# Optimization experiments

Measured on AMD Instinct MI355X. Metric: run time of the kernel, lower is better.

The kernel has to match this reference:

```python
import jax, jax.numpy as jnp
import numpy as np

B, S, DIM, H = 2, 2048, 1536, 12
HD = DIM // H  # 128
EPS = 1e-6


def setup_inputs() -> dict:
    key = jax.random.key(0)
    ks = jax.random.split(key, 6)
    x = jax.random.normal(ks[0], (B, S, DIM), dtype=jnp.float32)
    # RoPE rotation as (cos, sin) pairs: shape [S, 1, HD//2, 2]
    inv = 1.0 / (10000.0 ** (np.arange(0, HD, 2, dtype=np.float32) / HD))
    ang = np.arange(S, dtype=np.float32)[:, None] * inv[None, :]  # [S, HD//2]
    freqs = jnp.asarray(np.stack([np.cos(ang), np.sin(ang)], axis=-1))[:, None, :, :]
    def lin(k):
        return jax.random.normal(k, (DIM, DIM), dtype=jnp.float32) * 0.02
    wq, wk, wv, wo = lin(ks[1]), lin(ks[2]), lin(ks[3]), lin(ks[4])
    zb = jnp.zeros((DIM,), dtype=jnp.float32)
    ones = jnp.ones((DIM,), dtype=jnp.float32)
    return dict(x=x, freqs=freqs,
                wq=wq, bq=zb, wk=wk, bk=zb, wv=wv, bv=zb, wo=wo, bo=zb,
                gq=ones, gk=ones, timestep=500)


def reference(x, freqs, wq, bq, wk, bk, wv, bv, wo, bo, gq, gk, timestep):
    b, s, dim = x.shape

    def rms(z, g):
        zf = z.astype(jnp.float32)
        n = zf * jax.lax.rsqrt(jnp.mean(zf * zf, axis=-1, keepdims=True) + EPS)
        return n.astype(z.dtype) * g

    def rope(t):
        # [b,s,dim] -> [b,s,H,HD//2,2] pairs; complex multiply by freqs
        tp = t.reshape(b, s, H, HD // 2, 2)
        tr, ti = tp[..., 0], tp[..., 1]
        fr = freqs[None, ..., 0]  # [1,s,1,HD//2] broadcasts over batch & heads
        fi = freqs[None, ..., 1]
        out = jnp.stack([tr * fr - ti * fi, tr * fi + ti * fr], axis=-1)
        return out.reshape(b, s, dim)

    q = rope(rms(x @ wq.T + bq, gq))
    k = rope(rms(x @ wk.T + bk, gk))
    v = x @ wv.T + bv

    qh = q.reshape(b, s, H, HD).transpose(0, 2, 1, 3)
    kh = k.reshape(b, s, H, HD).transpose(0, 2, 1, 3)
    vh = v.reshape(b, s, H, HD).transpose(0, 2, 1, 3)
    scores = jnp.einsum('bhqd,bhkd->bhqk', qh, kh) / np.float32(np.sqrt(HD))
    attn = jax.nn.softmax(scores, axis=-1)
    out = jnp.einsum('bhqk,bhkd->bhqd', attn, vh)
    out = out.transpose(0, 2, 1, 3).reshape(b, s, dim)
    return out @ wo.T + bo
```

## Files before the change

kernel.cpp:

```cpp
#include <hip/hip_runtime.h>
#include <hip/hip_bf16.h>


#define BQ  2
#define SQ  2048
#define DIMQ 1536
#define HQ  12
#define HDQ 128
#define MTOK 4096
#define KDIM 1536

typedef __attribute__((ext_vector_type(8))) short short8;
typedef __attribute__((ext_vector_type(4))) float f32x4;
typedef __attribute__((ext_vector_type(16))) float f32x16;
typedef __attribute__((ext_vector_type(8))) unsigned short u16x8;

typedef __attribute__((address_space(1))) const void global_cvoid;
typedef __attribute__((address_space(3))) void lds_void;

__device__ __forceinline__ float bf2f(unsigned int u) {
    return __uint_as_float(u << 16);
}
__device__ __forceinline__ unsigned short f2bf(float f) {
    unsigned int u = __float_as_uint(f);
    u += 0x7fffu + ((u >> 16) & 1u);
    return (unsigned short)(u >> 16);
}
__device__ __forceinline__ void gload_lds16(const void* g, void* l) {
    __builtin_amdgcn_global_load_lds((global_cvoid*)g, (lds_void*)l, 16, 0, 0);
}
__device__ __forceinline__ unsigned int cvtpk_bf16(float lo, float hi) {
    unsigned int r;
    asm("v_cvt_pk_bf16_f32 %0, %1, %2" : "=v"(r) : "v"(lo), "v"(hi));
    return r;
}

#define VMCNT(n) asm volatile("s_waitcnt vmcnt(" #n ")" ::: "memory")
#define BARRIER() do { asm volatile("" ::: "memory"); \
                       __builtin_amdgcn_s_barrier();  \
                       asm volatile("" ::: "memory"); } while (0)

__global__ __launch_bounds__(256)
void cast_all(const float* __restrict__ x,
              const float* __restrict__ wq, const float* __restrict__ wk,
              const float* __restrict__ wv, const float* __restrict__ wo,
              unsigned short* __restrict__ Xb,
              unsigned short* __restrict__ Wqkv,
              unsigned short* __restrict__ Wob)
{
    const int NX = 1572864, NW = 589824;
    int i = blockIdx.x * blockDim.x + threadIdx.x;
    int stride = gridDim.x * blockDim.x;
    for (; i < NX + 4 * NW; i += stride) {
        const float* s; unsigned short* d; int off;
        if (i < NX) { s = x; d = Xb; off = i; }
        else {
            int j = i - NX;
            int seg = j / NW;
            off = j - seg * NW;
            s = (seg == 0) ? wq : (seg == 1) ? wk : (seg == 2) ? wv : wo;
            d = (seg < 3) ? (Wqkv + seg * 2359296) : Wob;
        }
        float4 v = ((const float4*)s)[off];
        unsigned short a = f2bf(v.x), b = f2bf(v.y), c = f2bf(v.z), e = f2bf(v.w);
        unsigned int lo = (unsigned int)a | ((unsigned int)b << 16);
        unsigned int hi = (unsigned int)c | ((unsigned int)e << 16);
        ((uint2*)d)[off] = make_uint2(lo, hi);
    }
}

template<int MODE>
__global__ __launch_bounds__(256)
void gemm_bt(const unsigned short* __restrict__ A,
             const unsigned short* __restrict__ Bm,
             unsigned short* __restrict__ oQ,
             unsigned short* __restrict__ oK,
             unsigned short* __restrict__ oV,
             const float* __restrict__ biasq,
             const float* __restrict__ biask,
             const float* __restrict__ biasv,
             float* __restrict__ oF,
             const float* __restrict__ biaso)
{
    __shared__ unsigned short ldsA[128 * 64];
    __shared__ unsigned short ldsB[128 * 64];
    const int m0 = blockIdx.x * 128;
    const int n0 = blockIdx.y * 128;
    const int t = threadIdx.x;
    const int lane = t & 63;
    const int wid = t >> 6;
    const int wr = (wid >> 1) * 64;
    const int wc = (wid & 1) * 64;
    const int lr = lane & 15;
    const int lk = lane >> 4;

    f32x4 acc[4][4] = {};

    #pragma unroll 1
    for (int kt = 0; kt < KDIM; kt += 64) {
        #pragma unroll
        for (int i = 0; i < 4; ++i) {
            const int off = i * 4096 + wid * 1024 + lane * 16;
            const int r = off >> 7;
            const int c = (off >> 4) & 7;
            const int csw = (c ^ (r & 7)) << 3;
            gload_lds16(A + (size_t)(m0 + r) * KDIM + kt + csw,
                        (char*)ldsA + i * 4096 + wid * 1024);
            gload_lds16(Bm + (size_t)(n0 + r) * KDIM + kt + csw,
                        (char*)ldsB + i * 4096 + wid * 1024);
        }
        __syncthreads();

        #pragma unroll
        for (int kk = 0; kk < 2; ++kk) {
            short8 af[4], bf[4];
            #pragma unroll
            for (int mi = 0; mi < 4; ++mi) {
                int row = wr + mi * 16 + lr;
                int ch = (kk * 4 + lk) ^ (row & 7);
                af[mi] = *(const short8*)((const char*)ldsA + row * 128 + ch * 16);
            }
            #pragma unroll
            for (int ni = 0; ni < 4; ++ni) {
                int row = wc + ni * 16 + lr;
                int ch = (kk * 4 + lk) ^ (row & 7);
                bf[ni] = *(const short8*)((const char*)ldsB + row * 128 + ch * 16);
            }
            #pragma unroll
            for (int mi = 0; mi < 4; ++mi)
                #pragma unroll
                for (int ni = 0; ni < 4; ++ni)
                    acc[mi][ni] = __builtin_amdgcn_mfma_f32_16x16x32_bf16(
                        af[mi], bf[ni], acc[mi][ni], 0, 0, 0);
        }
        __syncthreads();
    }

    if (MODE == 0) {
        const int seg = n0 / 1536;
        unsigned short* op = (seg == 0) ? oQ : (seg == 1 ? oK : oV);
        const float* bp = (seg == 0) ? biasq : (seg == 1 ? biask : biasv);
        const int nl0 = n0 - seg * 1536;
        #pragma unroll
        for (int mi = 0; mi < 4; ++mi)
            #pragma unroll
            for (int ni = 0; ni < 4; ++ni)
                #pragma unroll
                for (int j = 0; j < 4; ++j) {
                    int row = m0 + wr + mi * 16 + lk * 4 + j;
                    int col = nl0 + wc + ni * 16 + lr;
                    op[(size_t)row * 1536 + col] = f2bf(acc[mi][ni][j] + bp[col]);
                }
    } else {
        #pragma unroll
        for (int mi = 0; mi < 4; ++mi)
            #pragma unroll
            for (int ni = 0; ni < 4; ++ni)
                #pragma unroll
                for (int j = 0; j < 4; ++j) {
                    int row = m0 + wr + mi * 16 + lk * 4 + j;
                    int col = n0 + wc + ni * 16 + lr;
                    oF[(size_t)row * 1536 + col] = acc[mi][ni][j] + biaso[col];
                }
    }
}

__global__ __launch_bounds__(256)
void rmsnorm_rope(unsigned short* __restrict__ T,
                  const float* __restrict__ g,
                  const float* __restrict__ freqs)
{
    const int token = blockIdx.x;
    const int s = token & (SQ - 1);
    unsigned int* row = (unsigned int*)(T + (size_t)token * DIMQ);
    const int t = threadIdx.x;
    const int lane = t & 63, wid = t >> 6;

    float pr[3], pi[3];
    float ss = 0.f;
    #pragma unroll
    for (int q = 0; q < 3; ++q) {
        unsigned int v = row[t + q * 256];
        float a = bf2f(v & 0xffffu);
        float b = bf2f(v >> 16);
        pr[q] = a; pi[q] = b;
        ss += a * a + b * b;
    }
    ss += __shfl_xor(ss, 32); ss += __shfl_xor(ss, 16); ss += __shfl_xor(ss, 8);
    ss += __shfl_xor(ss, 4);  ss += __shfl_xor(ss, 2);  ss += __shfl_xor(ss, 1);
    __shared__ float red[4];
    if (lane == 0) red[wid] = ss;
    __syncthreads();
    float tot = red[0] + red[1] + red[2] + red[3];
    float sc = rsqrtf(tot * (1.0f / 1536.0f) + 1e-6f);

    #pragma unroll
    for (int q = 0; q < 3; ++q) {
        int p = t + q * 256;
        int ph = p & 63;
        float fr = freqs[s * 128 + ph * 2];
        float fi = freqs[s * 128 + ph * 2 + 1];
        float nr = pr[q] * sc * g[2 * p];
        float ni = pi[q] * sc * g[2 * p + 1];
        float outr = nr * fr - ni * fi;
        float outi = nr * fi + ni * fr;
        row[p] = (unsigned int)f2bf(outr) | ((unsigned int)f2bf(outi) << 16);
    }
}

__global__ __launch_bounds__(256)
void vtrans(const unsigned short* __restrict__ V, unsigned short* __restrict__ Vt)
{
    __shared__ unsigned short tile[64][72];
    const int s0 = blockIdx.x * 64;
    const int d0 = blockIdx.y * 64;
    const int bh = blockIdx.z;
    const int b = bh / HQ, h = bh % HQ;
    const int t = threadIdx.x;

    #pragma unroll
    for (int i = 0; i < 2; ++i) {
        int cid = i * 256 + t;
        int r = cid >> 3, c = cid & 7;
        u16x8 v = *(const u16x8*)(V + (size_t)(b * SQ + s0 + r) * DIMQ + h * HDQ + d0 + c * 8);
        #pragma unroll
        for (int e = 0; e < 8; ++e) tile[r][c * 8 + e] = v[e];
    }
    __syncthreads();
    #pragma unroll
    for (int i = 0; i < 2; ++i) {
        int cid = i * 256 + t;
        int rd = cid >> 3, c = cid & 7;
        u16x8 w;
        #pragma unroll
        for (int e = 0; e < 8; ++e) w[e] = tile[c * 8 + e][rd];
        *(u16x8*)(Vt + (size_t)(bh * HDQ + d0 + rd) * SQ + s0 + c * 8) = w;
    }
}

__global__ __launch_bounds__(128)
void attn(const unsigned short* __restrict__ Q,
          const unsigned short* __restrict__ Kb,
          const unsigned short* __restrict__ Vt,
          unsigned short* __restrict__ Ao)
{
    __shared__ char smem[49152];
    char* Kl0 = smem;
    char* Kl1 = smem + 16384;
    char* Vl  = smem + 32768;

    const int fid = blockIdx.x;
    const int xcd = fid & 7;
    const int slot = fid >> 3;
    const int bh = xcd * 3 + (slot >> 5);
    const int sblk = slot & 31;
    const int b = bh / HQ, h = bh % HQ;
    const int s0 = sblk * 64;

    const int t = threadIdx.x;
    const int lane = t & 63, wid = t >> 6;
    const int l31 = lane & 31, hi = lane >> 5;
    const float THR = 90.5f;
    const float CE = 0.12751879f;

    const unsigned short* Kbase = Kb + (size_t)(b * SQ) * DIMQ + h * HDQ;
    const unsigned short* Vbase = Vt + (size_t)(bh * HDQ) * SQ;

    short8 qf[8];
    {
        const int qrow = b * SQ + s0 + wid * 32 + l31;
        const unsigned short* qp = Q + (size_t)qrow * DIMQ + h * HDQ;
        #pragma unroll
        for (int kc = 0; kc < 8; ++kc)
            qf[kc] = *(const short8*)(qp + kc * 16 + hi * 8);
    }

    float mrun = -1e30f, lsum = 0.f;
    f32x16 oacc[4] = {};

    #pragma unroll
    for (int i = 0; i < 8; ++i) {
        const int off = i * 2048 + t * 16;
        int r = off >> 8, c = (off >> 4) & 15;
        gload_lds16(Kbase + (size_t)r * DIMQ + ((c ^ (r & 7)) << 3),
                    Kl0 + i * 2048 + wid * 1024);
    }

    char* kcur = Kl0;
    char* knxt = Kl1;

    #pragma unroll 1
    for (int kv0 = 0; kv0 < SQ; kv0 += 64) {
        #pragma unroll
        for (int i = 0; i < 8; ++i) {
            const int off = i * 2048 + t * 16;
            int r = off >> 7, c = (off >> 4) & 7;
            gload_lds16(Vbase + (size_t)r * SQ + kv0 + ((c ^ (r & 7)) << 3),
                        Vl + i * 2048 + wid * 1024);
        }
        asm volatile("" ::: "memory");
        const int kvn = (kv0 + 64 < SQ) ? kv0 + 64 : kv0;
        #pragma unroll
        for (int i = 0; i < 8; ++i) {
            const int off = i * 2048 + t * 16;
            int r = off >> 8, c = (off >> 4) & 15;
            gload_lds16(Kbase + (size_t)(kvn + r) * DIMQ + ((c ^ (r & 7)) << 3),
                        knxt + i * 2048 + wid * 1024);
        }

        VMCNT(16);
        BARRIER();

        f32x16 sacc[2] = {};
        __builtin_amdgcn_s_setprio(1);
        #pragma unroll
        for (int kvt = 0; kvt < 2; ++kvt) {
            const int krow = kvt * 32 + l31;
            const int rb = krow * 256;
            #pragma unroll
            for (int kc = 0; kc < 8; ++kc) {
                int ch = (kc * 2 + hi) ^ (krow & 7);
                short8 kf = *(const short8*)(kcur + rb + ch * 16);
                sacc[kvt] = __builtin_amdgcn_mfma_f32_32x32x16_bf16(kf, qf[kc], sacc[kvt], 0, 0, 0);
            }
        }
        __builtin_amdgcn_s_setprio(0);

        float mt[16];
        #pragma unroll
        for (int r = 0; r < 16; ++r) mt[r] = fmaxf(sacc[0][r], sacc[1][r]);
        #pragma unroll
        for (int s = 8; s > 0; s >>= 1)
            #pragma unroll
            for (int r = 0; r < 8; ++r)
                if (r < s) mt[r] = fmaxf(mt[r], mt[r + s]);
        float tm = mt[0];
        tm = fmaxf(tm, __shfl_xor(tm, 32));
        if (!__all(tm <= mrun + THR)) {
            float mnew = fmaxf(mrun, tm);
            float al = __builtin_amdgcn_exp2f((mrun - mnew) * CE);
            lsum *= al;
            #pragma unroll
            for (int dt = 0; dt < 4; ++dt)
                #pragma unroll
                for (int r = 0; r < 16; ++r) oacc[dt][r] *= al;
            mrun = mnew;
        }
        float rs = 0.f;
        #pragma unroll
        for (int kvt = 0; kvt < 2; ++kvt)
            #pragma unroll
            for (int r = 0; r < 16; ++r) {
                float p = __builtin_amdgcn_exp2f((sacc[kvt][r] - mrun) * CE);
                sacc[kvt][r] = p;
                rs += p;
            }
        rs += __shfl_xor(rs, 32);
        lsum += rs;

        VMCNT(8);
        BARRIER();

        __builtin_amdgcn_s_setprio(1);
        #pragma unroll
        for (int ks = 0; ks < 4; ++ks) {
            const int g = ks * 8;
            #define SV(f) (sacc[(f) >> 4][(f) & 15])
            unsigned int a0 = cvtpk_bf16(SV(g + 0), SV(g + 1));
            unsigned int a1 = cvtpk_bf16(SV(g + 2), SV(g + 3));
            unsigned int b0 = cvtpk_bf16(SV(g + 4), SV(g + 5));
            unsigned int b1 = cvtpk_bf16(SV(g + 6), SV(g + 7));
            #undef SV
            unsigned int xa0 = __shfl_xor(a0, 32);
            unsigned int xa1 = __shfl_xor(a1, 32);
            unsigned int xb0 = __shfl_xor(b0, 32);
            unsigned int xb1 = __shfl_xor(b1, 32);
            union { unsigned int w[4]; short8 v; } pf;
            pf.w[0] = hi ? xb0 : a0;
            pf.w[1] = hi ? xb1 : a1;
            pf.w[2] = hi ? b0 : xa0;
            pf.w[3] = hi ? b1 : xa1;
            #pragma unroll
            for (int dt = 0; dt < 4; ++dt) {
                const int drow = dt * 32 + l31;
                int ch = (ks * 2 + hi) ^ (drow & 7);
                short8 vf = *(const short8*)(Vl + drow * 128 + ch * 16);
                oacc[dt] = __builtin_amdgcn_mfma_f32_32x32x16_bf16(vf, pf.v, oacc[dt], 0, 0, 0);
            }
        }
        __builtin_amdgcn_s_setprio(0);

        BARRIER();

        char* tmp = kcur; kcur = knxt; knxt = tmp;
    }

    const float rls = 1.0f / lsum;
    char* Ot = smem + 32768 + wid * 8192;
    #pragma unroll
    for (int dt = 0; dt < 4; ++dt)
        #pragma unroll
        for (int rp = 0; rp < 8; ++rp) {
            const int r = 2 * rp;
            float v0 = oacc[dt][r] * rls;
            float v1 = oacc[dt][r + 1] * rls;
            int d = dt * 32 + (r & 3) + 8 * (r >> 2) + 4 * hi;
            unsigned int w = (unsigned int)f2bf(v0) | ((unsigned int)f2bf(v1) << 16);
            int addr = l31 * 256 + (((d >> 3) ^ (l31 & 7)) << 4) + (d & 7) * 2;
            *(unsigned int*)(Ot + addr) = w;
        }
    #pragma unroll
    for (int ii = 0; ii < 8; ++ii) {
        int task = ii * 64 + lane;
        int q = task >> 4, c = task & 15;
        u16x8 vv = *(const u16x8*)(Ot + q * 256 + ((c ^ (q & 7)) << 4));
        int tok = b * SQ + s0 + wid * 32 + q;
        *(u16x8*)(Ao + (size_t)tok * DIMQ + h * HDQ + c * 8) = vv;
    }
}

extern "C" void kernel_launch(void* const* d_in, const int* in_sizes, int n_in,
                              void* d_out, int out_size, void* d_ws, size_t ws_size,
                              hipStream_t stream) {
    (void)in_sizes; (void)n_in; (void)out_size; (void)ws_size;
    const float* x     = (const float*)d_in[0];
    const float* freqs = (const float*)d_in[1];
    const float* wq = (const float*)d_in[2];
    const float* bq = (const float*)d_in[3];
    const float* wk = (const float*)d_in[4];
    const float* bk = (const float*)d_in[5];
    const float* wv = (const float*)d_in[6];
    const float* bv = (const float*)d_in[7];
    const float* wo = (const float*)d_in[8];
    const float* bo = (const float*)d_in[9];
    const float* gq = (const float*)d_in[10];
    const float* gk = (const float*)d_in[11];
    float* out = (float*)d_out;

    char* w = (char*)d_ws;
    unsigned short* Xb   = (unsigned short*)(w);
    unsigned short* Wqkv = (unsigned short*)(w + 12582912);
    unsigned short* Wob  = (unsigned short*)(w + 26738688);
    unsigned short* Qb   = (unsigned short*)(w + 31457280);
    unsigned short* Kbuf = (unsigned short*)(w + 44040192);
    unsigned short* Vb   = (unsigned short*)(w + 56623104);
    unsigned short* Vt   = (unsigned short*)(w + 69206016);
    unsigned short* Ao   = Xb;

    cast_all<<<2048, 256, 0, stream>>>(x, wq, wk, wv, wo, Xb, Wqkv, Wob);

    gemm_bt<0><<<dim3(32, 36), 256, 0, stream>>>(
        Xb, Wqkv, Qb, Kbuf, Vb, bq, bk, bv, nullptr, nullptr);

    rmsnorm_rope<<<4096, 256, 0, stream>>>(Qb,   gq, freqs);
    rmsnorm_rope<<<4096, 256, 0, stream>>>(Kbuf, gk, freqs);
    vtrans<<<dim3(32, 2, 24), 256, 0, stream>>>(Vb, Vt);

    attn<<<768, 128, 0, stream>>>(Qb, Kbuf, Vt, Ao);

    gemm_bt<1><<<dim3(32, 12), 256, 0, stream>>>(
        Ao, Wob, nullptr, nullptr, nullptr, nullptr, nullptr, nullptr, out, bo);
}
```

Before: 277.9 us.

## Restructure attention to single-wave blocks with 32-key tiles and no barriers

The attention kernel now runs one 64-thread wavefront per block handling 32 query rows with 32-key KV tiles. Because each block has a single wave, all s_barrier calls are removed, leaving only vmcnt waits. The V tile gets a new swizzle layout, the exponent is computed as one fused multiply-add with a precomputed offset, and the QK accumulation is split across two accumulators. This removes inter-wave synchronisation and raises block count, but each block loads K/V tiles for only 32 queries, which doubles K/V global traffic per query and adds loop overhead.

```diff
diff --git a/kernel.cpp b/kernel.cpp
--- a/kernel.cpp
+++ b/kernel.cpp
@@ -36,9 +36,7 @@
 }
 
 #define VMCNT(n) asm volatile("s_waitcnt vmcnt(" #n ")" ::: "memory")
-#define BARRIER() do { asm volatile("" ::: "memory"); \
-                       __builtin_amdgcn_s_barrier();  \
-                       asm volatile("" ::: "memory"); } while (0)
+#define MEMFENCE() asm volatile("" ::: "memory")
 
 __global__ __launch_bounds__(256)
 void cast_all(const float* __restrict__ x,
@@ -238,104 +236,101 @@
     }
 }
 
-__global__ __launch_bounds__(128)
+__global__ __launch_bounds__(64, 2)
 void attn(const unsigned short* __restrict__ Q,
           const unsigned short* __restrict__ Kb,
           const unsigned short* __restrict__ Vt,
           unsigned short* __restrict__ Ao)
 {
-    __shared__ char smem[49152];
+    __shared__ char smem[24576];
     char* Kl0 = smem;
-    char* Kl1 = smem + 16384;
-    char* Vl  = smem + 32768;
+    char* Kl1 = smem + 8192;
+    char* Vl  = smem + 16384;
 
     const int fid = blockIdx.x;
     const int xcd = fid & 7;
     const int slot = fid >> 3;
-    const int bh = xcd * 3 + (slot >> 5);
-    const int sblk = slot & 31;
+    const int bh = xcd * 3 + (slot >> 6);
+    const int sblk = slot & 63;
     const int b = bh / HQ, h = bh % HQ;
-    const int s0 = sblk * 64;
-
-    const int t = threadIdx.x;
-    const int lane = t & 63, wid = t >> 6;
+    const int s0 = sblk * 32;
+
+    const int lane = threadIdx.x;
     const int l31 = lane & 31, hi = lane >> 5;
+    const float CE = 0.12751879f;
     const float THR = 90.5f;
-    const float CE = 0.12751879f;
 
     const unsigned short* Kbase = Kb + (size_t)(b * SQ) * DIMQ + h * HDQ;
     const unsigned short* Vbase = Vt + (size_t)(bh * HDQ) * SQ;
 
     short8 qf[8];
     {
-        const int qrow = b * SQ + s0 + wid * 32 + l31;
-        const unsigned short* qp = Q + (size_t)qrow * DIMQ + h * HDQ;
+        const unsigned short* qp = Q + (size_t)(b * SQ + s0 + l31) * DIMQ + h * HDQ;
         #pragma unroll
         for (int kc = 0; kc < 8; ++kc)
             qf[kc] = *(const short8*)(qp + kc * 16 + hi * 8);
     }
-
-    float mrun = -1e30f, lsum = 0.f;
-    f32x16 oacc[4] = {};
-
+    MEMFENCE();
     #pragma unroll
     for (int i = 0; i < 8; ++i) {
-        const int off = i * 2048 + t * 16;
+        const int off = i * 1024 + lane * 16;
         int r = off >> 8, c = (off >> 4) & 15;
-        gload_lds16(Kbase + (size_t)r * DIMQ + ((c ^ (r & 7)) << 3),
-                    Kl0 + i * 2048 + wid * 1024);
-    }
+        gload_lds16(Kbase + (size_t)r * DIMQ + ((c ^ (r & 7)) << 3), Kl0 + i * 1024);
+    }
+    VMCNT(8);
 
     char* kcur = Kl0;
     char* knxt = Kl1;
+    float mrun = -1e30f, lsum = 0.f, nm = 1e30f;
+    f32x16 oacc[4] = {};
 
     #pragma unroll 1
-    for (int kv0 = 0; kv0 < SQ; kv0 += 64) {
+    for (int kv0 = 0; kv0 < SQ; kv0 += 32) {
         #pragma unroll
         for (int i = 0; i < 8; ++i) {
-            const int off = i * 2048 + t * 16;
-            int r = off >> 7, c = (off >> 4) & 7;
-            gload_lds16(Vbase + (size_t)r * SQ + kv0 + ((c ^ (r & 7)) << 3),
-                        Vl + i * 2048 + wid * 1024);
-        }
-        asm volatile("" ::: "memory");
-        const int kvn = (kv0 + 64 < SQ) ? kv0 + 64 : kv0;
+            const int off = i * 1024 + lane * 16;
+            int r = off >> 6, c = (off >> 4) & 3;
+            gload_lds16(Vbase + (size_t)r * SQ + kv0 + ((c ^ ((r >> 1) & 3)) << 3),
+                        Vl + i * 1024);
+        }
+        MEMFENCE();
+        const int kvn = (kv0 + 32 < SQ) ? kv0 + 32 : kv0;
         #pragma unroll
         for (int i = 0; i < 8; ++i) {
-            const int off = i * 2048 + t * 16;
+            const int off = i * 1024 + lane * 16;
             int r = off >> 8, c = (off >> 4) & 15;
             gload_lds16(Kbase + (size_t)(kvn + r) * DIMQ + ((c ^ (r & 7)) << 3),
-                        knxt + i * 2048 + wid * 1024);
+                        knxt + i * 1024);
         }
 
         VMCNT(16);
-        BARRIER();
-
-        f32x16 sacc[2] = {};
-        __builtin_amdgcn_s_setprio(1);
-        #pragma unroll
-        for (int kvt = 0; kvt < 2; ++kvt) {
-            const int krow = kvt * 32 + l31;
-            const int rb = krow * 256;
-            #pragma unroll
-            for (int kc = 0; kc < 8; ++kc) {
-                int ch = (kc * 2 + hi) ^ (krow & 7);
-                short8 kf = *(const short8*)(kcur + rb + ch * 16);
-                sacc[kvt] = __builtin_amdgcn_mfma_f32_32x32x16_bf16(kf, qf[kc], sacc[kvt], 0, 0, 0);
-            }
-        }
-        __builtin_amdgcn_s_setprio(0);
-
-        float mt[16];
-        #pragma unroll
-        for (int r = 0; r < 16; ++r) mt[r] = fmaxf(sacc[0][r], sacc[1][r]);
-        #pragma unroll
-        for (int s = 8; s > 0; s >>= 1)
-            #pragma unroll
-            for (int r = 0; r < 8; ++r)
-                if (r < s) mt[r] = fmaxf(mt[r], mt[r + s]);
-        float tm = mt[0];
-        tm = fmaxf(tm, __shfl_xor(tm, 32));
+
+        f32x16 sa = {}, sb = {};
+        const int rb = l31 * 256;
+        const int rx = l31 & 7;
+        #pragma unroll
+        for (int kc = 0; kc < 4; ++kc) {
+            short8 kf = *(const short8*)(kcur + rb + (((kc * 2 + hi) ^ rx) << 4));
+            sa = __builtin_amdgcn_mfma_f32_32x32x16_bf16(kf, qf[kc], sa, 0, 0, 0);
+        }
+        #pragma unroll
+        for (int kc = 4; kc < 8; ++kc) {
+            short8 kf = *(const short8*)(kcur + rb + (((kc * 2 + hi) ^ rx) << 4));
+            sb = __builtin_amdgcn_mfma_f32_32x32x16_bf16(kf, qf[kc], sb, 0, 0, 0);
+        }
+        f32x16 s;
+        #pragma unroll
+        for (int r = 0; r < 16; ++r) s[r] = sa[r] + sb[r];
+
+        float mt[8];
+        #pragma unroll
+        for (int r = 0; r < 8; ++r) mt[r] = fmaxf(s[r], s[r + 8]);
+        #pragma unroll
+        for (int st = 4; st > 0; st >>= 1)
+            #pragma unroll
+            for (int r = 0; r < 4; ++r)
+                if (r < st) mt[r] = fmaxf(mt[r], mt[r + st]);
+        float tm = fmaxf(mt[0], __shfl_xor(mt[0], 32));
         if (!__all(tm <= mrun + THR)) {
             float mnew = fmaxf(mrun, tm);
             float al = __builtin_amdgcn_exp2f((mrun - mnew) * CE);
@@ -345,58 +340,48 @@
                 #pragma unroll
                 for (int r = 0; r < 16; ++r) oacc[dt][r] *= al;
             mrun = mnew;
+            nm = -mrun * CE;
         }
         float rs = 0.f;
         #pragma unroll
-        for (int kvt = 0; kvt < 2; ++kvt)
-            #pragma unroll
-            for (int r = 0; r < 16; ++r) {
-                float p = __builtin_amdgcn_exp2f((sacc[kvt][r] - mrun) * CE);
-                sacc[kvt][r] = p;
-                rs += p;
-            }
+        for (int r = 0; r < 16; ++r) {
+            float p = __builtin_amdgcn_exp2f(__builtin_fmaf(s[r], CE, nm));
+            s[r] = p; rs += p;
+        }
         rs += __shfl_xor(rs, 32);
         lsum += rs;
 
+        unsigned int A0 = cvtpk_bf16(s[0], s[1]),  A1 = cvtpk_bf16(s[2], s[3]);
+        unsigned int B0 = cvtpk_bf16(s[4], s[5]),  B1 = cvtpk_bf16(s[6], s[7]);
+        unsigned int C0 = cvtpk_bf16(s[8], s[9]),  C1 = cvtpk_bf16(s[10], s[11]);
+        unsigned int D0 = cvtpk_bf16(s[12], s[13]), D1 = cvtpk_bf16(s[14], s[15]);
+        unsigned int xA0 = __shfl_xor(A0, 32), xA1 = __shfl_xor(A1, 32);
+        unsigned int xB0 = __shfl_xor(B0, 32), xB1 = __shfl_xor(B1, 32);
+        unsigned int xC0 = __shfl_xor(C0, 32), xC1 = __shfl_xor(C1, 32);
+        unsigned int xD0 = __shfl_xor(D0, 32), xD1 = __shfl_xor(D1, 32);
+        union { unsigned int w[4]; short8 v; } pf0, pf1;
+        pf0.w[0] = hi ? xB0 : A0;  pf0.w[1] = hi ? xB1 : A1;
+        pf0.w[2] = hi ? B0 : xA0;  pf0.w[3] = hi ? B1 : xA1;
+        pf1.w[0] = hi ? xD0 : C0;  pf1.w[1] = hi ? xD1 : C1;
+        pf1.w[2] = hi ? D0 : xC0;  pf1.w[3] = hi ? D1 : xC1;
+
         VMCNT(8);
-        BARRIER();
-
-        __builtin_amdgcn_s_setprio(1);
-        #pragma unroll
-        for (int ks = 0; ks < 4; ++ks) {
-            const int g = ks * 8;
-            #define SV(f) (sacc[(f) >> 4][(f) & 15])
-            unsigned int a0 = cvtpk_bf16(SV(g + 0), SV(g + 1));
-            unsigned int a1 = cvtpk_bf16(SV(g + 2), SV(g + 3));
-            unsigned int b0 = cvtpk_bf16(SV(g + 4), SV(g + 5));
-            unsigned int b1 = cvtpk_bf16(SV(g + 6), SV(g + 7));
-            #undef SV
-            unsigned int xa0 = __shfl_xor(a0, 32);
-            unsigned int xa1 = __shfl_xor(a1, 32);
-            unsigned int xb0 = __shfl_xor(b0, 32);
-            unsigned int xb1 = __shfl_xor(b1, 32);
-            union { unsigned int w[4]; short8 v; } pf;
-            pf.w[0] = hi ? xb0 : a0;
-            pf.w[1] = hi ? xb1 : a1;
-            pf.w[2] = hi ? b0 : xa0;
-            pf.w[3] = hi ? b1 : xa1;
-            #pragma unroll
-            for (int dt = 0; dt < 4; ++dt) {
-                const int drow = dt * 32 + l31;
-                int ch = (ks * 2 + hi) ^ (drow & 7);
-                short8 vf = *(const short8*)(Vl + drow * 128 + ch * 16);
-                oacc[dt] = __builtin_amdgcn_mfma_f32_32x32x16_bf16(vf, pf.v, oacc[dt], 0, 0, 0);
-            }
-        }
-        __builtin_amdgcn_s_setprio(0);
-
-        BARRIER();
-
-        char* tmp = kcur; kcur = knxt; knxt = tmp;
+
+        #pragma unroll
+        for (int dt = 0; dt < 4; ++dt) {
+            const int drow = dt * 32 + l31;
+            const int sw = (drow >> 1) & 3;
+            short8 v0 = *(const short8*)(Vl + drow * 64 + ((hi ^ sw) << 4));
+            short8 v1 = *(const short8*)(Vl + drow * 64 + (((2 + hi) ^ sw) << 4));
+            oacc[dt] = __builtin_amdgcn_mfma_f32_32x32x16_bf16(v0, pf0.v, oacc[dt], 0, 0, 0);
+            oacc[dt] = __builtin_amdgcn_mfma_f32_32x32x16_bf16(v1, pf1.v, oacc[dt], 0, 0, 0);
+        }
+
+        char* tp = kcur; kcur = knxt; knxt = tp;
     }
 
     const float rls = 1.0f / lsum;
-    char* Ot = smem + 32768 + wid * 8192;
+    char* Ot = Vl;
     #pragma unroll
     for (int dt = 0; dt < 4; ++dt)
         #pragma unroll
@@ -414,7 +399,7 @@
         int task = ii * 64 + lane;
         int q = task >> 4, c = task & 15;
         u16x8 vv = *(const u16x8*)(Ot + q * 256 + ((c ^ (q & 7)) << 4));
-        int tok = b * SQ + s0 + wid * 32 + q;
+        int tok = b * SQ + s0 + q;
         *(u16x8*)(Ao + (size_t)tok * DIMQ + h * HDQ + c * 8) = vv;
     }
 }
@@ -456,7 +441,7 @@
     rmsnorm_rope<<<4096, 256, 0, stream>>>(Kbuf, gk, freqs);
     vtrans<<<dim3(32, 2, 24), 256, 0, stream>>>(Vb, Vt);
 
-    attn<<<768, 128, 0, stream>>>(Qb, Kbuf, Vt, Ao);
+    attn<<<1536, 64, 0, stream>>>(Qb, Kbuf, Vt, Ao);
 
     gemm_bt<1><<<dim3(32, 12), 256, 0, stream>>>(
         Ao, Wob, nullptr, nullptr, nullptr, nullptr, nullptr, nullptr, out, bo);
```

After: 255.4 us. -8.1%, faster.
